# Performance work log

Measured on AMD Instinct MI355X. Metric: run time of the kernel, lower is better.

## Reference

```python
import jax, jax.numpy as jnp
import numpy as np

V, T, DA, DS, KR, DU, KA = 64, 8192, 256, 256, 8, 64, 40
BETA_DET = 1.0
EPS = 1e-8


def _l2n(x):
    # torch F.normalize: x / max(||x||_2, 1e-12) along last dim
    n = jnp.linalg.norm(x, axis=-1, keepdims=True)
    return x / jnp.maximum(n, 1e-12)


def setup_inputs() -> dict:
    key = jax.random.key(0)
    ks = jax.random.split(key, 10)
    f32 = jnp.float32
    return {
        "h_aligned": jax.random.normal(ks[0], (V, T, DA), f32),
        "alpha": jax.random.uniform(ks[1], (V,), f32),
        "pi": jax.random.uniform(ks[2], (KR,), f32),
        "US": jax.random.normal(ks[3], (KR * DU,), f32),
        "Wc_w": 0.02 * jax.random.normal(ks[4], (DS, KR * DU), f32),
        "Wc_b": jnp.zeros((DS,), f32),
        "Ws_w": 0.02 * jax.random.normal(ks[5], (DS, KR * DU), f32),
        "Ws_b": jnp.zeros((DS,), f32),
        "det_w": 0.02 * jax.random.normal(ks[6], (1, DS), f32),
        "det_b": jnp.zeros((1,), f32),
        "cls_w": 0.02 * jax.random.normal(ks[7], (KA, DS), f32),
        "cls_b": jnp.zeros((KA,), f32),
        "Wwin_w": 0.02 * jax.random.normal(ks[8], (DS, DA), f32),
        "tau_c0": jnp.zeros((), f32),
        "lamU": jnp.asarray(0.1, f32),
        "lamC": jnp.asarray(0.1, f32),
        "lamP": jnp.asarray(0.1, f32),
        "lamPi": jnp.asarray(0.1, f32),
        "nu": jnp.zeros((), f32),
        "risk": jnp.zeros((), f32),
    }


def reference(h_aligned, alpha, pi, US, Wc_w, Wc_b, Ws_w, Ws_b, det_w, det_b,
              cls_w, cls_b, Wwin_w, tau_c0, lamU, lamC, lamP, lamPi, nu, risk):
    # SCD small heads
    zc = US @ Wc_w.T + Wc_b            # (ds,) -- computed as in original (unused downstream)
    zs = US @ Ws_w.T + Ws_b            # (ds,)
    s = zs @ det_w[0] + det_b[0]       # scalar detection score

    # tau_x from entropies
    C_alpha = 1.0 - (-(alpha * jnp.log(alpha + EPS)).sum()) / jnp.log(jnp.asarray(float(V), alpha.dtype))
    u_pi = (-(pi * jnp.log(pi + EPS)).sum()) / jnp.log(jnp.asarray(float(KR), pi.dtype))
    tau_x = tau_c0 - lamU * nu - lamC * C_alpha + lamP * risk + lamPi * u_pi

    p_det = jax.nn.sigmoid(BETA_DET * (s - tau_x))
    y_hat = jax.nn.sigmoid(zs @ cls_w.T + cls_b)   # (Ka,)

    # qpl_localize: per-window cosine score against normalized zs
    z_win = _l2n(jnp.einsum('vtd,sd->vts', h_aligned, Wwin_w))  # (V,T,ds)
    e = jnp.einsum('vts,s->vt', z_win, _l2n(zs))                # (V,T)
    E_view = e.mean(axis=1)                                     # (V,)
    r_view = -0.5 * alpha                                       # r0=0, beta_alpha=0.5

    # vectorized run-length interval detection (replaces python V*T loop):
    # starts[v,t]=True iff an interval begins at t; ends[v,t]=True iff one ends at t
    I = e >= r_view[:, None]                                    # (V,T) bool
    prev = jnp.pad(I[:, :-1], ((0, 0), (1, 0)))
    nxt = jnp.pad(I[:, 1:], ((0, 0), (0, 1)))
    starts = I & ~prev
    ends = I & ~nxt

    I_view = E_view >= r_view
    flag_unknown = (p_det >= 0.5) & (~I_view.any())
    return (p_det, tau_x, y_hat, e, E_view, r_view, I_view, starts, ends, flag_unknown)
```

## Files before the change

### kernel.cpp

```cpp
#include <hip/hip_runtime.h>
#include <math.h>

#define V 64
#define T 8192
#define DA 256
#define DS 256
#define KR 8
#define KA 40
#define KRDU 512

#define OUT_PDET   0
#define OUT_TAU    1
#define OUT_YHAT   2
#define OUT_E      42
#define OUT_EVIEW  524330
#define OUT_RVIEW  524394
#define OUT_IVIEW  524458
#define OUT_STARTS 524522
#define OUT_ENDS   1048810
#define OUT_FLAG   1573098

#define WS_W    0
#define WS_ESUM 256
#define WS_ZSN  320

typedef __attribute__((ext_vector_type(8))) short short8;
typedef __attribute__((ext_vector_type(4))) float f32x4;

__device__ __forceinline__ unsigned pack_bf16(float a, float b) {
    union { float f; unsigned u; } x, y; x.f = a; y.f = b;
    unsigned ua = (x.u + 0x7FFFu + ((x.u >> 16) & 1u)) >> 16;
    unsigned ub = (y.u + 0x7FFFu + ((y.u >> 16) & 1u)) & 0xFFFF0000u;
    return ua | ub;
}

__global__ __launch_bounds__(256) void head_kernel(
    const float* __restrict__ alpha, const float* __restrict__ pi,
    const float* __restrict__ US, const float* __restrict__ Ws_w,
    const float* __restrict__ Ws_b, const float* __restrict__ det_w,
    const float* __restrict__ det_b, const float* __restrict__ cls_w,
    const float* __restrict__ cls_b,
    const float* __restrict__ tau_c0, const float* __restrict__ lamU,
    const float* __restrict__ lamC, const float* __restrict__ lamP,
    const float* __restrict__ lamPi, const float* __restrict__ nu,
    const float* __restrict__ risk,
    float* __restrict__ out, float* __restrict__ ws)
{
    __shared__ float us[KRDU];
    __shared__ float zs[DS];
    __shared__ float red[256];
    const int tid = threadIdx.x;
    const int rr = tid >> 4;
    const int c  = tid & 15;

    us[tid]       = US[tid];
    us[tid + 256] = US[tid + 256];
    __syncthreads();

    for (int rg = 0; rg < 16; ++rg) {
        int row = rg * 16 + rr;
        const float4* wr = (const float4*)(Ws_w + (size_t)row * KRDU);
        float a = 0.0f;
        #pragma unroll
        for (int jj = 0; jj < 8; ++jj) {
            float4 w4 = wr[jj * 16 + c];
            int j0 = (jj * 16 + c) * 4;
            a += w4.x * us[j0] + w4.y * us[j0+1] + w4.z * us[j0+2] + w4.w * us[j0+3];
        }
        #pragma unroll
        for (int m = 8; m >= 1; m >>= 1) a += __shfl_xor(a, m);
        if (c == 0) zs[row] = a;
    }
    __syncthreads();
    float zv = zs[tid] + Ws_b[tid];
    __syncthreads();
    zs[tid] = zv;

    red[tid] = zv * det_w[tid];
    __syncthreads();
    for (int off = 128; off > 0; off >>= 1) { if (tid < off) red[tid] += red[tid+off]; __syncthreads(); }
    float s_det = red[0] + det_b[0];
    __syncthreads();

    red[tid] = zv * zv;
    __syncthreads();
    for (int off = 128; off > 0; off >>= 1) { if (tid < off) red[tid] += red[tid+off]; __syncthreads(); }
    float inv_n = 1.0f / fmaxf(sqrtf(red[0]), 1e-12f);
    __syncthreads();
    ws[WS_ZSN + tid] = zv * inv_n;

    float term = 0.0f;
    if (tid < V) { float a = alpha[tid]; term = -a * logf(a + 1e-8f); }
    red[tid] = term;
    __syncthreads();
    for (int off = 128; off > 0; off >>= 1) { if (tid < off) red[tid] += red[tid+off]; __syncthreads(); }
    float C_alpha = 1.0f - red[0] / logf((float)V);
    __syncthreads();

    term = 0.0f;
    if (tid < KR) { float p = pi[tid]; term = -p * logf(p + 1e-8f); }
    red[tid] = term;
    __syncthreads();
    for (int off = 128; off > 0; off >>= 1) { if (tid < off) red[tid] += red[tid+off]; __syncthreads(); }
    float u_pi = red[0] / logf((float)KR);
    __syncthreads();

    float tau = tau_c0[0] - lamU[0]*nu[0] - lamC[0]*C_alpha + lamP[0]*risk[0] + lamPi[0]*u_pi;
    if (tid == 0) {
        out[OUT_TAU]  = tau;
        out[OUT_PDET] = 1.0f / (1.0f + expf(-(s_det - tau)));
    }

    for (int rg = 0; rg < 3; ++rg) {
        int row = rg * 16 + rr;
        float a = 0.0f;
        if (row < KA) {
            const float4* cr4 = (const float4*)(cls_w + (size_t)row * DS);
            #pragma unroll
            for (int jj = 0; jj < 4; ++jj) {
                float4 w4 = cr4[jj * 16 + c];
                int j0 = (jj * 16 + c) * 4;
                a += w4.x * zs[j0] + w4.y * zs[j0+1] + w4.z * zs[j0+2] + w4.w * zs[j0+3];
            }
        }
        #pragma unroll
        for (int m = 8; m >= 1; m >>= 1) a += __shfl_xor(a, m);
        if (c == 0 && row < KA) out[OUT_YHAT + row] = 1.0f / (1.0f + expf(-(a + cls_b[row])));
    }

    ws[WS_W + tid] = 0.0f;
    if (tid < V) {
        out[OUT_RVIEW + tid] = -0.5f * alpha[tid];
        ws[WS_ESUM + tid] = 0.0f;
    }
}

__global__ __launch_bounds__(256) void wvec_kernel(const float* __restrict__ Wwin,
                                                   float* __restrict__ ws)
{
    __shared__ float zl[16];
    const int b = blockIdx.x;
    const int tid = threadIdx.x;
    if (tid < 16) zl[tid] = ws[WS_ZSN + b * 16 + tid];
    __syncthreads();
    float a = 0.0f;
    #pragma unroll
    for (int s = 0; s < 16; ++s) a += Wwin[(size_t)(b * 16 + s) * DA + tid] * zl[s];
    atomicAdd(&ws[WS_W + tid], a);
}

#define HROWB 264

__global__ __launch_bounds__(256, 2) void escore_kernel(
    const float* __restrict__ h, const float* __restrict__ Wwin,
    float* __restrict__ ws, float* __restrict__ out)
{
    __shared__ unsigned short hsb[2][16 * HROWB];
    __shared__ float numbuf[2][16];
    __shared__ float nrmbuf[2][4][16];

    const int tid  = threadIdx.x;
    const int lane = tid & 63;
    const int wv   = tid >> 6;
    const int ln15 = lane & 15;
    const int lq   = lane >> 4;

    short8 Wf[4][8];
    {
        const int nbase = wv * 64 + ln15;
        #pragma unroll
        for (int st = 0; st < 4; ++st) {
            const float* wrow = Wwin + (size_t)(nbase + st * 16) * DA + lq * 8;
            #pragma unroll
            for (int kk = 0; kk < 8; ++kk) {
                float4 f0 = *(const float4*)(wrow + kk * 32);
                float4 f1 = *(const float4*)(wrow + kk * 32 + 4);
                union { short8 s; unsigned u[4]; } pk;
                pk.u[0] = pack_bf16(f0.x, f0.y);
                pk.u[1] = pack_bf16(f0.z, f0.w);
                pk.u[2] = pack_bf16(f1.x, f1.y);
                pk.u[3] = pack_bf16(f1.z, f1.w);
                Wf[st][kk] = pk.s;
            }
        }
    }
    const float4 wq = *(const float4*)(ws + WS_W + 4 * lane);

    const long rowbase0 = (long)blockIdx.x * 1024;
    float esum = 0.0f;

    for (int tile = 0; tile < 64; ++tile) {
        const int p = tile & 1;
        const long rowbase = rowbase0 + tile * 16;

        const float4* hg = (const float4*)(h + rowbase * DA);
        float4 f[4];
        #pragma unroll
        for (int i = 0; i < 4; ++i) f[i] = hg[tid + 256 * i];

        #pragma unroll
        for (int i = 0; i < 4; ++i) {
            float np = f[i].x * wq.x + f[i].y * wq.y + f[i].z * wq.z + f[i].w * wq.w;
            #pragma unroll
            for (int m = 32; m >= 1; m >>= 1) np += __shfl_xor(np, m);
            if (lane == 0) numbuf[p][wv + 4 * i] = np;
        }
        #pragma unroll
        for (int i = 0; i < 4; ++i) {
            unsigned u0 = pack_bf16(f[i].x, f[i].y);
            unsigned u1 = pack_bf16(f[i].z, f[i].w);
            *(uint2*)&hsb[p][(wv + 4 * i) * HROWB + lane * 4] = make_uint2(u0, u1);
        }
        __syncthreads();

        f32x4 acc[4];
        #pragma unroll
        for (int st = 0; st < 4; ++st) acc[st] = (f32x4){0.f, 0.f, 0.f, 0.f};
        #pragma unroll
        for (int kk = 0; kk < 8; ++kk) {
            short8 af = *(const short8*)&hsb[p][ln15 * HROWB + kk * 32 + lq * 8];
            acc[0] = __builtin_amdgcn_mfma_f32_16x16x32_bf16(af, Wf[0][kk], acc[0], 0, 0, 0);
            acc[1] = __builtin_amdgcn_mfma_f32_16x16x32_bf16(af, Wf[1][kk], acc[1], 0, 0, 0);
            acc[2] = __builtin_amdgcn_mfma_f32_16x16x32_bf16(af, Wf[2][kk], acc[2], 0, 0, 0);
            acc[3] = __builtin_amdgcn_mfma_f32_16x16x32_bf16(af, Wf[3][kk], acc[3], 0, 0, 0);
        }
        float nr2[4];
        #pragma unroll
        for (int reg = 0; reg < 4; ++reg)
            nr2[reg] = acc[0][reg]*acc[0][reg] + acc[1][reg]*acc[1][reg]
                     + acc[2][reg]*acc[2][reg] + acc[3][reg]*acc[3][reg];
        #pragma unroll
        for (int m = 1; m <= 8; m <<= 1) {
            nr2[0] += __shfl_xor(nr2[0], m);
            nr2[1] += __shfl_xor(nr2[1], m);
            nr2[2] += __shfl_xor(nr2[2], m);
            nr2[3] += __shfl_xor(nr2[3], m);
        }
        if (ln15 == 0) {
            #pragma unroll
            for (int reg = 0; reg < 4; ++reg) nrmbuf[p][wv][lq * 4 + reg] = nr2[reg];
        }
        __syncthreads();

        if (tid < 16) {
            float nn = nrmbuf[p][0][tid] + nrmbuf[p][1][tid] + nrmbuf[p][2][tid] + nrmbuf[p][3][tid];
            float e = numbuf[p][tid] / fmaxf(sqrtf(nn), 1e-12f);
            out[OUT_E + rowbase + tid] = e;
            esum += e;
        }
    }

    if (tid < 64) {
        float s = (tid < 16) ? esum : 0.0f;
        #pragma unroll
        for (int m = 1; m <= 8; m <<= 1) s += __shfl_xor(s, m);
        if (tid == 0) atomicAdd(&ws[WS_ESUM + (blockIdx.x >> 3)], s);
    }
}

__global__ __launch_bounds__(256) void fixup_kernel(
    const float* __restrict__ h, const float* __restrict__ Wwin,
    const float* __restrict__ alpha, const float* __restrict__ ws,
    float* __restrict__ out)
{
    const int tid  = threadIdx.x;
    const int lane = tid & 63;
    const long row = (long)blockIdx.x * 256 + tid;
    const float e  = out[OUT_E + row];
    const float r  = -0.5f * alpha[row >> 13];
    bool flag = fabsf(e - r) < 2e-3f;
    unsigned long long mask = __ballot(flag);
    while (mask) {
        int t = __ffsll((unsigned long long)mask) - 1;
        mask &= mask - 1;
        const long frow = (long)blockIdx.x * 256 + (tid & ~63) + t;
        const float* hr = h + frow * DA;
        float z0 = 0.f, z1 = 0.f, z2 = 0.f, z3 = 0.f;
        const float* wp = Wwin + (size_t)(lane * 4) * DA;
        for (int d = 0; d < DA; ++d) {
            float hd = hr[d];
            z0 += hd * wp[d];
            z1 += hd * wp[d + DA];
            z2 += hd * wp[d + 2 * DA];
            z3 += hd * wp[d + 3 * DA];
        }
        float nrm = z0*z0 + z1*z1 + z2*z2 + z3*z3;
        float num = 0.f;
        #pragma unroll
        for (int j = 0; j < 4; ++j) num += hr[lane + 64 * j] * ws[WS_W + lane + 64 * j];
        #pragma unroll
        for (int m = 32; m >= 1; m >>= 1) { nrm += __shfl_xor(nrm, m); num += __shfl_xor(num, m); }
        if (lane == 0) out[OUT_E + frow] = num / fmaxf(sqrtf(nrm), 1e-12f);
    }
}

__global__ void finalize_kernel(const float* __restrict__ alpha,
                                const float* __restrict__ ws,
                                float* __restrict__ out)
{
    int v = threadIdx.x;
    float E = ws[WS_ESUM + v] * (1.0f / 8192.0f);
    out[OUT_EVIEW + v] = E;
    float r = -0.5f * alpha[v];
    bool Iv = (E >= r);
    out[OUT_IVIEW + v] = Iv ? 1.0f : 0.0f;
    unsigned long long bal = __ballot(Iv);
    if (v == 0) {
        float p = out[OUT_PDET];
        out[OUT_FLAG] = ((p >= 0.5f) && (bal == 0ULL)) ? 1.0f : 0.0f;
    }
}

__global__ __launch_bounds__(256) void intervals_kernel(
    const float* __restrict__ alpha, float* __restrict__ out)
{
    int idx = blockIdx.x * 256 + threadIdx.x;
    int v = idx >> 13;
    int t = idx & (T - 1);
    const float* e = out + OUT_E;
    float r = -0.5f * alpha[v];
    bool Ii = (e[idx] >= r);
    bool Ip = (t > 0)     && (e[idx - 1] >= r);
    bool In = (t < T - 1) && (e[idx + 1] >= r);
    out[OUT_STARTS + idx] = (Ii && !Ip) ? 1.0f : 0.0f;
    out[OUT_ENDS   + idx] = (Ii && !In) ? 1.0f : 0.0f;
}

extern "C" void kernel_launch(void* const* d_in, const int* in_sizes, int n_in,
                              void* d_out, int out_size, void* d_ws, size_t ws_size,
                              hipStream_t stream)
{
    const float* h      = (const float*)d_in[0];
    const float* alpha  = (const float*)d_in[1];
    const float* pi     = (const float*)d_in[2];
    const float* US     = (const float*)d_in[3];
    const float* Ws_w   = (const float*)d_in[6];
    const float* Ws_b   = (const float*)d_in[7];
    const float* det_w  = (const float*)d_in[8];
    const float* det_b  = (const float*)d_in[9];
    const float* cls_w  = (const float*)d_in[10];
    const float* cls_b  = (const float*)d_in[11];
    const float* Wwin   = (const float*)d_in[12];
    const float* tau_c0 = (const float*)d_in[13];
    const float* lamU   = (const float*)d_in[14];
    const float* lamC   = (const float*)d_in[15];
    const float* lamP   = (const float*)d_in[16];
    const float* lamPi  = (const float*)d_in[17];
    const float* nu     = (const float*)d_in[18];
    const float* risk   = (const float*)d_in[19];
    float* out = (float*)d_out;
    float* ws  = (float*)d_ws;

    head_kernel<<<1, 256, 0, stream>>>(alpha, pi, US, Ws_w, Ws_b, det_w, det_b,
                                       cls_w, cls_b, tau_c0, lamU, lamC,
                                       lamP, lamPi, nu, risk, out, ws);
    wvec_kernel<<<16, 256, 0, stream>>>(Wwin, ws);
    escore_kernel<<<512, 256, 0, stream>>>(h, Wwin, ws, out);
    fixup_kernel<<<(V * T) / 256, 256, 0, stream>>>(h, Wwin, alpha, ws, out);
    finalize_kernel<<<1, 64, 0, stream>>>(alpha, ws, out);
    intervals_kernel<<<(V * T) / 256, 256, 0, stream>>>(alpha, out);
}
```

Before: 1.226 ms.

## Prefetch h tiles, compute cosine numerator from MFMA output, compact fixup list

The escore kernel now loads the next 16-row tile of h into registers while the MFMAs for the current tile run. It drops the separate fp32 numerator reduction and instead dots the MFMA output with the normalized zs. Per-tile partial norms and numerators are kept in shared memory so the division, output writes and view sum happen once per block, with one barrier per tile instead of two. Rows whose score lies near the threshold, within a widened margin, are appended to a global list that a 512-block fixup kernel recomputes in fp32, with a full-scan fallback if the list overflows. This removes the full-tensor ballot scan, but the numerator now carries bf16 rounding error, which the wider margin is meant to absorb.

```diff
diff --git a/kernel.cpp b/kernel.cpp
--- a/kernel.cpp
+++ b/kernel.cpp
@@ -23,6 +23,12 @@
 #define WS_W    0
 #define WS_ESUM 256
 #define WS_ZSN  320
+#define WS_CNT  576
+#define WS_LIST 640
+
+#define CAP    65536
+#define MARGIN 4e-3f
+#define HROWB  264
 
 typedef __attribute__((ext_vector_type(8))) short short8;
 typedef __attribute__((ext_vector_type(4))) float f32x4;
@@ -44,7 +50,7 @@
     const float* __restrict__ lamC, const float* __restrict__ lamP,
     const float* __restrict__ lamPi, const float* __restrict__ nu,
     const float* __restrict__ risk,
-    float* __restrict__ out, float* __restrict__ ws)
+    float* __restrict__ out, float* __restrict__ ws, int* __restrict__ wsi)
 {
     __shared__ float us[KRDU];
     __shared__ float zs[DS];
@@ -109,6 +115,7 @@
     if (tid == 0) {
         out[OUT_TAU]  = tau;
         out[OUT_PDET] = 1.0f / (1.0f + expf(-(s_det - tau)));
+        wsi[WS_CNT]   = 0;
     }
 
     for (int rg = 0; rg < 3; ++rg) {
@@ -149,15 +156,15 @@
     atomicAdd(&ws[WS_W + tid], a);
 }
 
-#define HROWB 264
-
 __global__ __launch_bounds__(256, 2) void escore_kernel(
     const float* __restrict__ h, const float* __restrict__ Wwin,
-    float* __restrict__ ws, float* __restrict__ out)
+    const float* __restrict__ alpha,
+    float* __restrict__ ws, int* __restrict__ wsi, float* __restrict__ out)
 {
     __shared__ unsigned short hsb[2][16 * HROWB];
-    __shared__ float numbuf[2][16];
-    __shared__ float nrmbuf[2][4][16];
+    __shared__ float part_n[4][1024];
+    __shared__ float part_u[4][1024];
+    __shared__ float red[4];
 
     const int tid  = threadIdx.x;
     const int lane = tid & 63;
@@ -184,27 +191,24 @@
             }
         }
     }
-    const float4 wq = *(const float4*)(ws + WS_W + 4 * lane);
-
+    float zl[4];
+    #pragma unroll
+    for (int st = 0; st < 4; ++st) zl[st] = ws[WS_ZSN + wv * 64 + st * 16 + ln15];
+
+    const int view = blockIdx.x >> 3;
+    const float rv = -0.5f * alpha[view];
     const long rowbase0 = (long)blockIdx.x * 1024;
-    float esum = 0.0f;
+
+    float4 f[4];
+    {
+        const float4* hg = (const float4*)(h + rowbase0 * DA);
+        #pragma unroll
+        for (int i = 0; i < 4; ++i) f[i] = hg[tid + 256 * i];
+    }
 
     for (int tile = 0; tile < 64; ++tile) {
         const int p = tile & 1;
-        const long rowbase = rowbase0 + tile * 16;
-
-        const float4* hg = (const float4*)(h + rowbase * DA);
-        float4 f[4];
-        #pragma unroll
-        for (int i = 0; i < 4; ++i) f[i] = hg[tid + 256 * i];
-
-        #pragma unroll
-        for (int i = 0; i < 4; ++i) {
-            float np = f[i].x * wq.x + f[i].y * wq.y + f[i].z * wq.z + f[i].w * wq.w;
-            #pragma unroll
-            for (int m = 32; m >= 1; m >>= 1) np += __shfl_xor(np, m);
-            if (lane == 0) numbuf[p][wv + 4 * i] = np;
-        }
+
         #pragma unroll
         for (int i = 0; i < 4; ++i) {
             unsigned u0 = pack_bf16(f[i].x, f[i].y);
@@ -212,6 +216,13 @@
             *(uint2*)&hsb[p][(wv + 4 * i) * HROWB + lane * 4] = make_uint2(u0, u1);
         }
         __syncthreads();
+
+        {
+            int nt = (tile < 63) ? tile + 1 : 63;
+            const float4* ng = (const float4*)(h + (rowbase0 + (long)nt * 16) * DA);
+            #pragma unroll
+            for (int i = 0; i < 4; ++i) f[i] = ng[tid + 256 * i];
+        }
 
         f32x4 acc[4];
         #pragma unroll
@@ -224,73 +235,123 @@
             acc[2] = __builtin_amdgcn_mfma_f32_16x16x32_bf16(af, Wf[2][kk], acc[2], 0, 0, 0);
             acc[3] = __builtin_amdgcn_mfma_f32_16x16x32_bf16(af, Wf[3][kk], acc[3], 0, 0, 0);
         }
-        float nr2[4];
-        #pragma unroll
-        for (int reg = 0; reg < 4; ++reg)
-            nr2[reg] = acc[0][reg]*acc[0][reg] + acc[1][reg]*acc[1][reg]
-                     + acc[2][reg]*acc[2][reg] + acc[3][reg]*acc[3][reg];
+
+        float nr[4], nu[4];
+        #pragma unroll
+        for (int reg = 0; reg < 4; ++reg) {
+            nr[reg] = acc[0][reg]*acc[0][reg] + acc[1][reg]*acc[1][reg]
+                    + acc[2][reg]*acc[2][reg] + acc[3][reg]*acc[3][reg];
+            nu[reg] = acc[0][reg]*zl[0] + acc[1][reg]*zl[1]
+                    + acc[2][reg]*zl[2] + acc[3][reg]*zl[3];
+        }
         #pragma unroll
         for (int m = 1; m <= 8; m <<= 1) {
-            nr2[0] += __shfl_xor(nr2[0], m);
-            nr2[1] += __shfl_xor(nr2[1], m);
-            nr2[2] += __shfl_xor(nr2[2], m);
-            nr2[3] += __shfl_xor(nr2[3], m);
+            #pragma unroll
+            for (int reg = 0; reg < 4; ++reg) {
+                nr[reg] += __shfl_xor(nr[reg], m);
+                nu[reg] += __shfl_xor(nu[reg], m);
+            }
         }
         if (ln15 == 0) {
-            #pragma unroll
-            for (int reg = 0; reg < 4; ++reg) nrmbuf[p][wv][lq * 4 + reg] = nr2[reg];
-        }
-        __syncthreads();
-
-        if (tid < 16) {
-            float nn = nrmbuf[p][0][tid] + nrmbuf[p][1][tid] + nrmbuf[p][2][tid] + nrmbuf[p][3][tid];
-            float e = numbuf[p][tid] / fmaxf(sqrtf(nn), 1e-12f);
-            out[OUT_E + rowbase + tid] = e;
-            esum += e;
-        }
-    }
-
-    if (tid < 64) {
-        float s = (tid < 16) ? esum : 0.0f;
-        #pragma unroll
-        for (int m = 1; m <= 8; m <<= 1) s += __shfl_xor(s, m);
-        if (tid == 0) atomicAdd(&ws[WS_ESUM + (blockIdx.x >> 3)], s);
-    }
+            *(float4*)&part_n[wv][tile * 16 + lq * 4] = make_float4(nr[0], nr[1], nr[2], nr[3]);
+            *(float4*)&part_u[wv][tile * 16 + lq * 4] = make_float4(nu[0], nu[1], nu[2], nu[3]);
+        }
+    }
+    __syncthreads();
+
+    float esum = 0.0f;
+    #pragma unroll
+    for (int j = 0; j < 4; ++j) {
+        int r = j * 256 + tid;
+        float nn = part_n[0][r] + part_n[1][r] + part_n[2][r] + part_n[3][r];
+        float uu = part_u[0][r] + part_u[1][r] + part_u[2][r] + part_u[3][r];
+        float e = uu / fmaxf(sqrtf(nn), 1e-12f);
+        out[OUT_E + rowbase0 + r] = e;
+        esum += e;
+        if (fabsf(e - rv) < MARGIN) {
+            int idx = atomicAdd(&wsi[WS_CNT], 1);
+            if (idx < CAP) wsi[WS_LIST + idx] = (int)(rowbase0 + r);
+        }
+    }
+    #pragma unroll
+    for (int m = 1; m <= 32; m <<= 1) esum += __shfl_xor(esum, m);
+    if (lane == 0) red[wv] = esum;
+    __syncthreads();
+    if (tid == 0) atomicAdd(&ws[WS_ESUM + view], red[0] + red[1] + red[2] + red[3]);
 }
 
 __global__ __launch_bounds__(256) void fixup_kernel(
     const float* __restrict__ h, const float* __restrict__ Wwin,
     const float* __restrict__ alpha, const float* __restrict__ ws,
-    float* __restrict__ out)
-{
+    const int* __restrict__ wsi, float* __restrict__ out)
+{
+    __shared__ float hrow[DA];
+    __shared__ float red[8];
     const int tid  = threadIdx.x;
     const int lane = tid & 63;
-    const long row = (long)blockIdx.x * 256 + tid;
-    const float e  = out[OUT_E + row];
-    const float r  = -0.5f * alpha[row >> 13];
-    bool flag = fabsf(e - r) < 2e-3f;
-    unsigned long long mask = __ballot(flag);
-    while (mask) {
-        int t = __ffsll((unsigned long long)mask) - 1;
-        mask &= mask - 1;
-        const long frow = (long)blockIdx.x * 256 + (tid & ~63) + t;
-        const float* hr = h + frow * DA;
+    const int wv   = tid >> 6;
+    const int cnt  = wsi[WS_CNT];
+    const int m    = cnt < CAP ? cnt : CAP;
+
+    for (int i = blockIdx.x; i < m; i += gridDim.x) {
+        const int row = wsi[WS_LIST + i];
+        hrow[tid] = h[(size_t)row * DA + tid];
+        __syncthreads();
+        const float4* wr = (const float4*)(Wwin + (size_t)tid * DA);
+        const float4* h4 = (const float4*)hrow;
         float z0 = 0.f, z1 = 0.f, z2 = 0.f, z3 = 0.f;
-        const float* wp = Wwin + (size_t)(lane * 4) * DA;
-        for (int d = 0; d < DA; ++d) {
-            float hd = hr[d];
-            z0 += hd * wp[d];
-            z1 += hd * wp[d + DA];
-            z2 += hd * wp[d + 2 * DA];
-            z3 += hd * wp[d + 3 * DA];
-        }
-        float nrm = z0*z0 + z1*z1 + z2*z2 + z3*z3;
-        float num = 0.f;
-        #pragma unroll
-        for (int j = 0; j < 4; ++j) num += hr[lane + 64 * j] * ws[WS_W + lane + 64 * j];
-        #pragma unroll
-        for (int m = 32; m >= 1; m >>= 1) { nrm += __shfl_xor(nrm, m); num += __shfl_xor(num, m); }
-        if (lane == 0) out[OUT_E + frow] = num / fmaxf(sqrtf(nrm), 1e-12f);
+        #pragma unroll 4
+        for (int j = 0; j < 64; j += 4) {
+            float4 a, b;
+            a = wr[j];   b = h4[j];   z0 += a.x*b.x + a.y*b.y + a.z*b.z + a.w*b.w;
+            a = wr[j+1]; b = h4[j+1]; z1 += a.x*b.x + a.y*b.y + a.z*b.z + a.w*b.w;
+            a = wr[j+2]; b = h4[j+2]; z2 += a.x*b.x + a.y*b.y + a.z*b.z + a.w*b.w;
+            a = wr[j+3]; b = h4[j+3]; z3 += a.x*b.x + a.y*b.y + a.z*b.z + a.w*b.w;
+        }
+        float zz  = (z0 + z1) + (z2 + z3);
+        float nrm = zz * zz;
+        float num = hrow[tid] * ws[WS_W + tid];
+        #pragma unroll
+        for (int s = 1; s <= 32; s <<= 1) { nrm += __shfl_xor(nrm, s); num += __shfl_xor(num, s); }
+        if (lane == 0) { red[wv] = nrm; red[4 + wv] = num; }
+        __syncthreads();
+        if (tid == 0) {
+            float nn = red[0] + red[1] + red[2] + red[3];
+            float uu = red[4] + red[5] + red[6] + red[7];
+            out[OUT_E + row] = uu / fmaxf(sqrtf(nn), 1e-12f);
+        }
+        __syncthreads();
+    }
+
+    if (cnt > CAP) {
+        for (long i = blockIdx.x; i < (long)V * T; i += gridDim.x) {
+            float r = -0.5f * alpha[i >> 13];
+            if (fabsf(out[OUT_E + i] - r) >= MARGIN) continue;
+            hrow[tid] = h[(size_t)i * DA + tid];
+            __syncthreads();
+            const float4* wr = (const float4*)(Wwin + (size_t)tid * DA);
+            const float4* h4 = (const float4*)hrow;
+            float z0 = 0.f, z1 = 0.f, z2 = 0.f, z3 = 0.f;
+            for (int j = 0; j < 64; j += 4) {
+                float4 a, b;
+                a = wr[j];   b = h4[j];   z0 += a.x*b.x + a.y*b.y + a.z*b.z + a.w*b.w;
+                a = wr[j+1]; b = h4[j+1]; z1 += a.x*b.x + a.y*b.y + a.z*b.z + a.w*b.w;
+                a = wr[j+2]; b = h4[j+2]; z2 += a.x*b.x + a.y*b.y + a.z*b.z + a.w*b.w;
+                a = wr[j+3]; b = h4[j+3]; z3 += a.x*b.x + a.y*b.y + a.z*b.z + a.w*b.w;
+            }
+            float zz  = (z0 + z1) + (z2 + z3);
+            float nrm = zz * zz;
+            float num = hrow[tid] * ws[WS_W + tid];
+            for (int s = 1; s <= 32; s <<= 1) { nrm += __shfl_xor(nrm, s); num += __shfl_xor(num, s); }
+            if (lane == 0) { red[wv] = nrm; red[4 + wv] = num; }
+            __syncthreads();
+            if (tid == 0) {
+                float nn = red[0] + red[1] + red[2] + red[3];
+                float uu = red[4] + red[5] + red[6] + red[7];
+                out[OUT_E + i] = uu / fmaxf(sqrtf(nn), 1e-12f);
+            }
+            __syncthreads();
+        }
     }
 }
 
@@ -350,13 +411,14 @@
     const float* risk   = (const float*)d_in[19];
     float* out = (float*)d_out;
     float* ws  = (float*)d_ws;
+    int*   wsi = (int*)d_ws;
 
     head_kernel<<<1, 256, 0, stream>>>(alpha, pi, US, Ws_w, Ws_b, det_w, det_b,
                                        cls_w, cls_b, tau_c0, lamU, lamC,
-                                       lamP, lamPi, nu, risk, out, ws);
+                                       lamP, lamPi, nu, risk, out, ws, wsi);
     wvec_kernel<<<16, 256, 0, stream>>>(Wwin, ws);
-    escore_kernel<<<512, 256, 0, stream>>>(h, Wwin, ws, out);
-    fixup_kernel<<<(V * T) / 256, 256, 0, stream>>>(h, Wwin, alpha, ws, out);
+    escore_kernel<<<512, 256, 0, stream>>>(h, Wwin, alpha, ws, wsi, out);
+    fixup_kernel<<<512, 256, 0, stream>>>(h, Wwin, alpha, ws, wsi, out);
     finalize_kernel<<<1, 64, 0, stream>>>(alpha, ws, out);
     intervals_kernel<<<(V * T) / 256, 256, 0, stream>>>(alpha, out);
 }
```

Result: faster. 1.023 ms (-16.5%).
